# Kernel optimization log

Hardware: AMD Instinct MI355X
Metric: run time of the kernel (lower is better)

The kernel has to match this reference:

```python
import jax, jax.numpy as jnp
import numpy as np

N, E, F_IN = 50000, 1_600_000, 256
HID, HEADS, NCLS = 8, 8, 16  # conv1: 8 heads x 8 dims (concat=64); conv2: 1 head -> 16 classes


def setup_inputs() -> dict:
    key = jax.random.key(0)
    ks = jax.random.split(key, 11)
    x = jax.random.normal(ks[0], (N, F_IN), dtype=jnp.float32)
    edge_index = jax.random.randint(ks[1], (2, E), 0, N, dtype=jnp.int32)
    s1 = 1.0 / np.sqrt(F_IN)
    W1 = jax.random.normal(ks[2], (F_IN, HEADS * HID), jnp.float32) * s1
    a_src1 = jax.random.normal(ks[3], (HEADS, HID), jnp.float32) * 0.1
    a_dst1 = jax.random.normal(ks[4], (HEADS, HID), jnp.float32) * 0.1
    b1 = jnp.zeros((HEADS * HID,), jnp.float32)
    s2 = 1.0 / np.sqrt(HEADS * HID)
    W2 = jax.random.normal(ks[5], (HEADS * HID, NCLS), jnp.float32) * s2
    a_src2 = jax.random.normal(ks[6], (1, NCLS), jnp.float32) * 0.1
    a_dst2 = jax.random.normal(ks[7], (1, NCLS), jnp.float32) * 0.1
    b2 = jnp.zeros((NCLS,), jnp.float32)
    return {"x": x, "edge_index": edge_index, "W1": W1, "a_src1": a_src1,
            "a_dst1": a_dst1, "b1": b1, "W2": W2, "a_src2": a_src2,
            "a_dst2": a_dst2, "b2": b2}


def _gat_conv(x, W, a_src, a_dst, bias, src, dst, n, heads, ch, concat):
    # per-head linear transform: [n, heads, ch]
    h = (x @ W).reshape(n, heads, ch)
    # additive attention logits per node, per head
    al_s = jnp.einsum('nhc,hc->nh', h, a_src)
    al_d = jnp.einsum('nhc,hc->nh', h, a_dst)
    e = jax.nn.leaky_relu(al_s[src] + al_d[dst], 0.2)  # [E_tot, heads]
    # segment softmax grouped by destination node (self-loops guarantee non-empty segments)
    m = jax.ops.segment_max(e, dst, num_segments=n)
    ex = jnp.exp(e - m[dst])
    den = jax.ops.segment_sum(ex, dst, num_segments=n)
    alpha = ex / den[dst]  # [E_tot, heads]
    # scatter-aggregate weighted neighbor features
    out = jax.ops.segment_sum(h[src] * alpha[:, :, None], dst, num_segments=n)
    out = out.reshape(n, heads * ch) if concat else out.mean(axis=1)
    return out + bias


def reference(x, edge_index, W1, a_src1, a_dst1, b1, W2, a_src2, a_dst2, b2):
    # add self-loops (PyG GATConv default)
    loops = jnp.arange(N, dtype=edge_index.dtype)
    src = jnp.concatenate([edge_index[0], loops])
    dst = jnp.concatenate([edge_index[1], loops])
    h = _gat_conv(x, W1, a_src1, a_dst1, b1, src, dst, N, HEADS, HID, True)
    h = jax.nn.elu(h)
    out = _gat_conv(h, W2, a_src2, a_dst2, b2, src, dst, N, 1, NCLS, False)
    return jax.nn.log_softmax(out, axis=1)
```

## Files before the change

### kernel.cpp

```cpp
#include <hip/hip_runtime.h>
#include <hip/hip_fp16.h>

#define NN   50000
#define FIN  256
#define C1   64
#define NH   8
#define NC   16
#define NE   1600000
#define NTOT (NE + NN)

#define CH   256
#define EPC  ((NTOT + CH - 1) / CH)
#define NCB  196
#define GB1  ((NN + 63) / 64)

typedef _Float16 half8 __attribute__((ext_vector_type(8)));
typedef _Float16 half4 __attribute__((ext_vector_type(4)));
typedef float f32x4 __attribute__((ext_vector_type(4)));

#define OFF_H1H   0
#define OFF_H2H   1600000
#define OFF_ALS2  2000000
#define OFF_ALD2  2050000
#define OFF_STAGE 3200000
#define OFF_ALS1  6400000
#define OFF_ALD1  6800000
#define OFF_HM    7200000
#define OFF_BASEK 7251000
#define OFF_BBASE 7302000
#define OFF_OFFS  7302400
#define OFF_SRC   7352500

__global__ __launch_bounds__(256) void k_g1rh(const float* __restrict__ x,
                                              const float* __restrict__ W1,
                                              const float* __restrict__ as1,
                                              const float* __restrict__ ad1,
                                              __half* __restrict__ h1h,
                                              float* __restrict__ als,
                                              float* __restrict__ ald,
                                              const int* __restrict__ ei,
                                              int* __restrict__ H) {
    __shared__ _Float16 wsT[64][264];
    __shared__ _Float16 xs[64][40];
    __shared__ int lh[NCB];
    const int tid = threadIdx.x;

    if (blockIdx.x >= GB1) {
        int k = blockIdx.x - GB1;
        for (int i = tid; i < NCB; i += 256) lh[i] = 0;
        __syncthreads();
        int e0 = k * EPC, e1 = min(e0 + EPC, NTOT);
        for (int e = e0 + tid; e < e1; e += 256) {
            int d = (e < NE) ? ei[NE + e] : (e - NE);
            atomicAdd(&lh[d >> 8], 1);
        }
        __syncthreads();
        for (int i = tid; i < NCB; i += 256) H[k * NCB + i] = lh[i];
        return;
    }

    const int r0 = blockIdx.x * 64;
    {
        int c = tid & 63, kb = tid >> 6;
        #pragma unroll
        for (int j = 0; j < 8; ++j) {
            int k8 = kb + 4 * j;
            half8 hv;
            #pragma unroll
            for (int u = 0; u < 8; ++u)
                hv[u] = (_Float16)W1[(size_t)(k8 * 8 + u) * C1 + c];
            *(half8*)(&wsT[c][k8 * 8]) = hv;
        }
    }

    const int lane = tid & 63;
    const int wv   = tid >> 6;
    const int colb = lane & 15;
    const int rgrp = lane >> 4;
    f32x4 acc[4] = {};
    const int srow = tid >> 2;
    const int sq   = tid & 3;
    for (int k0 = 0; k0 < FIN; k0 += 32) {
        __syncthreads();
        {
            int grow = r0 + srow;
            float4 v0 = make_float4(0.f,0.f,0.f,0.f), v1 = v0;
            if (grow < NN) {
                const float4* xp = (const float4*)(&x[(size_t)grow * FIN + k0 + sq * 8]);
                v0 = xp[0]; v1 = xp[1];
            }
            half8 hv;
            hv[0]=(_Float16)v0.x; hv[1]=(_Float16)v0.y; hv[2]=(_Float16)v0.z; hv[3]=(_Float16)v0.w;
            hv[4]=(_Float16)v1.x; hv[5]=(_Float16)v1.y; hv[6]=(_Float16)v1.z; hv[7]=(_Float16)v1.w;
            *(half8*)(&xs[srow][sq * 8]) = hv;
        }
        __syncthreads();
        half8 a = *(half8*)(&xs[wv * 16 + colb][rgrp * 8]);
        #pragma unroll
        for (int ct = 0; ct < 4; ++ct) {
            half8 b = *(half8*)(&wsT[ct * 16 + colb][k0 + rgrp * 8]);
            acc[ct] = __builtin_amdgcn_mfma_f32_16x16x32_f16(a, b, acc[ct], 0, 0, 0);
        }
    }

    float a_s[4], a_d[4];
    #pragma unroll
    for (int ct = 0; ct < 4; ++ct) { a_s[ct] = as1[ct * 16 + colb]; a_d[ct] = ad1[ct * 16 + colb]; }
    #pragma unroll
    for (int j = 0; j < 4; ++j) {
        int row = r0 + wv * 16 + rgrp * 4 + j;
        bool rv = row < NN;
        #pragma unroll
        for (int ct = 0; ct < 4; ++ct) {
            if (rv) h1h[(size_t)row * C1 + ct * 16 + colb] = __float2half(acc[ct][j]);
            float p = acc[ct][j] * a_s[ct];
            p += __shfl_xor(p, 1); p += __shfl_xor(p, 2); p += __shfl_xor(p, 4);
            float q = acc[ct][j] * a_d[ct];
            q += __shfl_xor(q, 1); q += __shfl_xor(q, 2); q += __shfl_xor(q, 4);
            if (rv && (lane & 7) == 0) {
                int head = ct * 2 + (colb >> 3);
                als[row * NH + head] = p;
                ald[row * NH + head] = q;
            }
        }
    }
}

__global__ __launch_bounds__(256) void k_rsA(const int* __restrict__ H,
                                             int* __restrict__ basek,
                                             int* __restrict__ btot) {
    __shared__ int sc[CH];
    int b = blockIdx.x, t = threadIdx.x;
    int v = H[t * NCB + b];
    sc[t] = v;
    __syncthreads();
    for (int s = 1; s < CH; s <<= 1) {
        int u = (t >= s) ? sc[t - s] : 0;
        __syncthreads();
        sc[t] += u;
        __syncthreads();
    }
    basek[b * CH + t] = sc[t] - v;
    if (t == CH - 1) btot[b] = sc[t];
}

__global__ __launch_bounds__(64) void k_rsB(int* __restrict__ btot,
                                            int* __restrict__ bbase,
                                            int* __restrict__ offs) {
    if (threadIdx.x == 0) {
        int run = 0;
        for (int b = 0; b < NCB; ++b) {
            bbase[b] = run;
            run += btot[b];
        }
        bbase[NCB] = run;
        offs[NN] = NTOT;
    }
}

__global__ __launch_bounds__(256) void k_rscatter(const int* __restrict__ ei,
                                                  const int* __restrict__ basek,
                                                  const int* __restrict__ bbase,
                                                  int* __restrict__ stage) {
    __shared__ int lcur[NCB];
    int k = blockIdx.x;
    for (int i = threadIdx.x; i < NCB; i += 256)
        lcur[i] = bbase[i] + basek[i * CH + k];
    __syncthreads();
    int e0 = k * EPC, e1 = min(e0 + EPC, NTOT);
    for (int e = e0 + threadIdx.x; e < e1; e += 256) {
        int s, d;
        if (e < NE) { s = ei[e]; d = ei[NE + e]; }
        else        { s = e - NE; d = s; }
        int pos = atomicAdd(&lcur[d >> 8], 1);
        stage[pos] = (s << 8) | (d & 255);
    }
}

__global__ __launch_bounds__(256) void k_fsort(const int* __restrict__ stage,
                                               const int* __restrict__ bbase,
                                               int* __restrict__ offs,
                                               int* __restrict__ ssrc) {
    __shared__ int lc[256];
    __shared__ int ls[256];
    __shared__ int lcur[256];
    int b = blockIdx.x, t = threadIdx.x;
    int base = bbase[b];
    int n = bbase[b + 1] - base;
    lc[t] = 0;
    __syncthreads();
    const int* sp = &stage[base];
    for (int i = t; i < n; i += 256) atomicAdd(&lc[sp[i] & 255], 1);
    __syncthreads();
    int v = lc[t];
    ls[t] = v;
    __syncthreads();
    for (int s = 1; s < 256; s <<= 1) {
        int u = (t >= s) ? ls[t - s] : 0;
        __syncthreads();
        ls[t] += u;
        __syncthreads();
    }
    int excl = ls[t] - v;
    int d = b * 256 + t;
    if (d < NN) offs[d] = base + excl;
    lcur[t] = base + excl;
    __syncthreads();
    for (int i = t; i < n; i += 256) {
        int u = sp[i];
        int pos = atomicAdd(&lcur[u & 255], 1);
        ssrc[pos] = u >> 8;
    }
}

__global__ __launch_bounds__(256) void k_agg1(const int* __restrict__ offs,
                                              const int* __restrict__ src,
                                              const __half* __restrict__ h1h,
                                              const float* __restrict__ als,
                                              const float* __restrict__ ald,
                                              const float* __restrict__ b1,
                                              const float* __restrict__ W2,
                                              const float* __restrict__ as2,
                                              const float* __restrict__ ad2,
                                              __half* __restrict__ h2h,
                                              float* __restrict__ als2,
                                              float* __restrict__ ald2) {
    __shared__ float lds_w2[C1][17];
    __shared__ float lds_g[4][C1];
    int tid = threadIdx.x;
    #pragma unroll
    for (int i = tid; i < C1 * NC; i += 256) lds_w2[i >> 4][i & 15] = W2[i];
    __syncthreads();

    int wv = tid >> 6;
    int d = blockIdx.x * 4 + wv;
    if (d >= NN) return;
    const int l  = tid & 63;
    const int q  = l >> 4, lc = l & 15;
    const int hg = lc >> 1;
    const int sub = l >> 3, hw = l & 7;
    const int lane_a = (q << 3) | hg;
    const int lane_b = lane_a + 32;
    int beg = offs[d], end = offs[d + 1];
    float aldv = ald[d * NH + hw];
    f32x4 acc = {0.f, 0.f, 0.f, 0.f};
    float den = 0.f;

    for (int r = beg; r < end; r += 16) {
        int e0 = r + sub, e1 = e0 + 8;
        bool v0 = e0 < end, v1 = e1 < end;
        int s0 = src[v0 ? e0 : end - 1];
        int s1 = src[v1 ? e1 : end - 1];
        float lg0 = als[s0 * NH + hw] + aldv;
        float lg1 = als[s1 * NH + hw] + aldv;
        lg0 = lg0 > 0.f ? lg0 : 0.2f * lg0;
        lg1 = lg1 > 0.f ? lg1 : 0.2f * lg1;
        float w0 = v0 ? __expf(lg0) : 0.f;
        float w1 = v1 ? __expf(lg1) : 0.f;
        #pragma unroll
        for (int i = 0; i < 4; ++i) {
            int srcl = (i & 1) ? lane_b : lane_a;
            int sv   = __shfl((i < 2) ? s0 : s1, srcl);
            float wvv= __shfl((i < 2) ? w0 : w1, srcl);
            half4 hv = *(const half4*)(&h1h[(size_t)sv * C1 + 4 * lc]);
            acc[0] += wvv * (float)hv[0];
            acc[1] += wvv * (float)hv[1];
            acc[2] += wvv * (float)hv[2];
            acc[3] += wvv * (float)hv[3];
            den += wvv;
        }
    }
    #pragma unroll
    for (int k = 0; k < 4; ++k) {
        acc[k] += __shfl_xor(acc[k], 16);
        acc[k] += __shfl_xor(acc[k], 32);
    }
    den += __shfl_xor(den, 16);
    den += __shfl_xor(den, 32);

    float g[4];
    #pragma unroll
    for (int k = 0; k < 4; ++k) {
        float o = acc[k] / den + b1[4 * lc + k];
        g[k] = o > 0.f ? o : (__expf(o) - 1.f);
    }
    if (q == 0) *(float4*)(&lds_g[wv][4 * lc]) = make_float4(g[0], g[1], g[2], g[3]);
    float h2p = 0.f;
    #pragma unroll
    for (int m = 0; m < 16; ++m)
        h2p += lds_g[wv][q * 16 + m] * lds_w2[q * 16 + m][lc];
    h2p += __shfl_xor(h2p, 16);
    h2p += __shfl_xor(h2p, 32);
    if (l < 16) h2h[(size_t)d * NC + lc] = __float2half(h2p);
    float ps = h2p * as2[lc], pd = h2p * ad2[lc];
    ps += __shfl_xor(ps, 1); ps += __shfl_xor(ps, 2);
    ps += __shfl_xor(ps, 4); ps += __shfl_xor(ps, 8);
    pd += __shfl_xor(pd, 1); pd += __shfl_xor(pd, 2);
    pd += __shfl_xor(pd, 4); pd += __shfl_xor(pd, 8);
    if (l == 0) { als2[d] = ps; ald2[d] = pd; }
}

__global__ __launch_bounds__(256) void k_agg2(const int* __restrict__ offs,
                                              const int* __restrict__ src,
                                              const __half* __restrict__ h2h,
                                              const float* __restrict__ als2,
                                              const float* __restrict__ ald2,
                                              const float* __restrict__ b2,
                                              float* __restrict__ out) {
    int d = blockIdx.x * 16 + (threadIdx.x >> 4);
    if (d >= NN) return;
    int c = threadIdx.x & 15;
    int beg = offs[d], end = offs[d + 1];
    float aldv = ald2[d];
    float acc = 0.f, den = 0.f;
    for (int r = beg; r < end; r += 4) {
        int e1 = r + 1, e2 = r + 2, e3 = r + 3;
        bool v1 = e1 < end, v2 = e2 < end, v3 = e3 < end;
        int s0 = src[r];
        int s1 = src[v1 ? e1 : end - 1];
        int s2 = src[v2 ? e2 : end - 1];
        int s3 = src[v3 ? e3 : end - 1];
        float l0 = als2[s0] + aldv;
        float l1 = als2[s1] + aldv;
        float l2 = als2[s2] + aldv;
        float l3 = als2[s3] + aldv;
        l0 = l0 > 0.f ? l0 : 0.2f * l0;
        l1 = l1 > 0.f ? l1 : 0.2f * l1;
        l2 = l2 > 0.f ? l2 : 0.2f * l2;
        l3 = l3 > 0.f ? l3 : 0.2f * l3;
        float w0 = __expf(l0);
        float w1 = v1 ? __expf(l1) : 0.f;
        float w2 = v2 ? __expf(l2) : 0.f;
        float w3 = v3 ? __expf(l3) : 0.f;
        float f0 = __half2float(h2h[(size_t)s0 * NC + c]);
        float f1 = __half2float(h2h[(size_t)s1 * NC + c]);
        float f2 = __half2float(h2h[(size_t)s2 * NC + c]);
        float f3 = __half2float(h2h[(size_t)s3 * NC + c]);
        acc += w0 * f0 + w1 * f1 + w2 * f2 + w3 * f3;
        den += w0 + w1 + w2 + w3;
    }
    float o = acc / den + b2[c];
    float m = o;
    #pragma unroll
    for (int w = 1; w < 16; w <<= 1) m = fmaxf(m, __shfl_xor(m, w));
    float ex = __expf(o - m);
    float sm = ex;
    #pragma unroll
    for (int w = 1; w < 16; w <<= 1) sm += __shfl_xor(sm, w);
    out[(size_t)d * NC + c] = o - m - __logf(sm);
}

extern "C" void kernel_launch(void* const* d_in, const int* in_sizes, int n_in,
                              void* d_out, int out_size, void* d_ws, size_t ws_size,
                              hipStream_t stream) {
    const float* x   = (const float*)d_in[0];
    const int*   ei  = (const int*)  d_in[1];
    const float* W1  = (const float*)d_in[2];
    const float* as1 = (const float*)d_in[3];
    const float* ad1 = (const float*)d_in[4];
    const float* b1  = (const float*)d_in[5];
    const float* W2  = (const float*)d_in[6];
    const float* as2 = (const float*)d_in[7];
    const float* ad2 = (const float*)d_in[8];
    const float* b2  = (const float*)d_in[9];
    float* ws  = (float*)d_ws;
    float* out = (float*)d_out;

    __half* h1h = (__half*)(ws + OFF_H1H);
    __half* h2h = (__half*)(ws + OFF_H2H);
    float* als1 = ws + OFF_ALS1;
    float* ald1 = ws + OFF_ALD1;
    float* als2 = ws + OFF_ALS2;
    float* ald2 = ws + OFF_ALD2;
    int* H      = (int*)(ws + OFF_HM);
    int* basek  = (int*)(ws + OFF_BASEK);
    int* bbase  = (int*)(ws + OFF_BBASE);
    int* offs   = (int*)(ws + OFF_OFFS);
    int* ssrc   = (int*)(ws + OFF_SRC);
    int* stage  = (int*)(ws + OFF_STAGE);

    k_g1rh    <<<GB1 + CH,       256, 0, stream>>>(x, W1, as1, ad1, h1h, als1, ald1, ei, H);
    k_rsA     <<<NCB,            256, 0, stream>>>(H, basek, bbase + NCB + 2 );
    k_rsB     <<<1,               64, 0, stream>>>(bbase + NCB + 2, bbase, offs);
    k_rscatter<<<CH,             256, 0, stream>>>(ei, basek, bbase, stage);
    k_fsort   <<<NCB,            256, 0, stream>>>(stage, bbase, offs, ssrc);
    k_agg1    <<<(NN + 3) / 4,   256, 0, stream>>>(offs, ssrc, h1h, als1, ald1, b1,
                                                   W2, as2, ad2, h2h, als2, ald2);
    k_agg2    <<<(NN + 15) / 16, 256, 0, stream>>>(offs, ssrc, h2h, als2, ald2, b2, out);
}
```

Measured before the change: 142.7 us.

## Split layer-2 GEMM out of agg1 and stage full x tile in LDS

The layer-1 aggregation kernel no longer computes the layer-2 projection. It writes ELU activations in fp16 to a new buffer, and a separate k_gemm2 kernel computes h2 and the layer-2 attention logits. The first GEMM kernel now loads the whole 64x256 x tile into LDS up front instead of looping over k-chunks with two barriers each. This trims LDS use and barriers in agg1 and removes per-iteration syncs in the GEMM, but adds an extra launch plus an activation round trip through memory. It also raises LDS per block in k_g1rh, which can lower occupancy.

```diff
diff --git a/kernel.cpp b/kernel.cpp
--- a/kernel.cpp
+++ b/kernel.cpp
@@ -19,10 +19,11 @@
 typedef float f32x4 __attribute__((ext_vector_type(4)));
 
 #define OFF_H1H   0
-#define OFF_H2H   1600000
-#define OFF_ALS2  2000000
-#define OFF_ALD2  2050000
+#define OFF_G1H   1600000
 #define OFF_STAGE 3200000
+#define OFF_H2H   3200000
+#define OFF_ALS2  3600000
+#define OFF_ALD2  3650000
 #define OFF_ALS1  6400000
 #define OFF_ALD1  6800000
 #define OFF_HM    7200000
@@ -41,11 +42,11 @@
                                               const int* __restrict__ ei,
                                               int* __restrict__ H) {
     __shared__ _Float16 wsT[64][264];
-    __shared__ _Float16 xs[64][40];
-    __shared__ int lh[NCB];
+    __shared__ _Float16 xs[64][264];
     const int tid = threadIdx.x;
 
     if (blockIdx.x >= GB1) {
+        __shared__ int lh[NCB];
         int k = blockIdx.x - GB1;
         for (int i = tid; i < NCB; i += 256) lh[i] = 0;
         __syncthreads();
@@ -72,33 +73,35 @@
             *(half8*)(&wsT[c][k8 * 8]) = hv;
         }
     }
+    {
+        int row = tid >> 2, cb = (tid & 3) * 64;
+        int grow = r0 + row;
+        #pragma unroll
+        for (int j = 0; j < 8; ++j) {
+            float4 v0 = make_float4(0.f,0.f,0.f,0.f), v1 = v0;
+            if (grow < NN) {
+                const float4* xp = (const float4*)(&x[(size_t)grow * FIN + cb + j * 8]);
+                v0 = xp[0]; v1 = xp[1];
+            }
+            half8 hv;
+            hv[0]=(_Float16)v0.x; hv[1]=(_Float16)v0.y; hv[2]=(_Float16)v0.z; hv[3]=(_Float16)v0.w;
+            hv[4]=(_Float16)v1.x; hv[5]=(_Float16)v1.y; hv[6]=(_Float16)v1.z; hv[7]=(_Float16)v1.w;
+            *(half8*)(&xs[row][cb + j * 8]) = hv;
+        }
+    }
+    __syncthreads();
 
     const int lane = tid & 63;
     const int wv   = tid >> 6;
     const int colb = lane & 15;
     const int rgrp = lane >> 4;
     f32x4 acc[4] = {};
-    const int srow = tid >> 2;
-    const int sq   = tid & 3;
-    for (int k0 = 0; k0 < FIN; k0 += 32) {
-        __syncthreads();
-        {
-            int grow = r0 + srow;
-            float4 v0 = make_float4(0.f,0.f,0.f,0.f), v1 = v0;
-            if (grow < NN) {
-                const float4* xp = (const float4*)(&x[(size_t)grow * FIN + k0 + sq * 8]);
-                v0 = xp[0]; v1 = xp[1];
-            }
-            half8 hv;
-            hv[0]=(_Float16)v0.x; hv[1]=(_Float16)v0.y; hv[2]=(_Float16)v0.z; hv[3]=(_Float16)v0.w;
-            hv[4]=(_Float16)v1.x; hv[5]=(_Float16)v1.y; hv[6]=(_Float16)v1.z; hv[7]=(_Float16)v1.w;
-            *(half8*)(&xs[srow][sq * 8]) = hv;
-        }
-        __syncthreads();
-        half8 a = *(half8*)(&xs[wv * 16 + colb][rgrp * 8]);
+    #pragma unroll
+    for (int s = 0; s < 8; ++s) {
+        half8 a = *(half8*)(&xs[wv * 16 + colb][s * 32 + rgrp * 8]);
         #pragma unroll
         for (int ct = 0; ct < 4; ++ct) {
-            half8 b = *(half8*)(&wsT[ct * 16 + colb][k0 + rgrp * 8]);
+            half8 b = *(half8*)(&wsT[ct * 16 + colb][s * 32 + rgrp * 8]);
             acc[ct] = __builtin_amdgcn_mfma_f32_16x16x32_f16(a, b, acc[ct], 0, 0, 0);
         }
     }
@@ -219,23 +222,10 @@
                                               const float* __restrict__ als,
                                               const float* __restrict__ ald,
                                               const float* __restrict__ b1,
-                                              const float* __restrict__ W2,
-                                              const float* __restrict__ as2,
-                                              const float* __restrict__ ad2,
-                                              __half* __restrict__ h2h,
-                                              float* __restrict__ als2,
-                                              float* __restrict__ ald2) {
-    __shared__ float lds_w2[C1][17];
-    __shared__ float lds_g[4][C1];
-    int tid = threadIdx.x;
-    #pragma unroll
-    for (int i = tid; i < C1 * NC; i += 256) lds_w2[i >> 4][i & 15] = W2[i];
-    __syncthreads();
-
-    int wv = tid >> 6;
-    int d = blockIdx.x * 4 + wv;
+                                              _Float16* __restrict__ g1h) {
+    int d = blockIdx.x * 4 + (threadIdx.x >> 6);
     if (d >= NN) return;
-    const int l  = tid & 63;
+    const int l  = threadIdx.x & 63;
     const int q  = l >> 4, lc = l & 15;
     const int hg = lc >> 1;
     const int sub = l >> 3, hw = l & 7;
@@ -277,32 +267,51 @@
     }
     den += __shfl_xor(den, 16);
     den += __shfl_xor(den, 32);
-
-    float g[4];
-    #pragma unroll
-    for (int k = 0; k < 4; ++k) {
-        float o = acc[k] / den + b1[4 * lc + k];
-        g[k] = o > 0.f ? o : (__expf(o) - 1.f);
-    }
-    if (q == 0) *(float4*)(&lds_g[wv][4 * lc]) = make_float4(g[0], g[1], g[2], g[3]);
-    float h2p = 0.f;
-    #pragma unroll
-    for (int m = 0; m < 16; ++m)
-        h2p += lds_g[wv][q * 16 + m] * lds_w2[q * 16 + m][lc];
-    h2p += __shfl_xor(h2p, 16);
-    h2p += __shfl_xor(h2p, 32);
-    if (l < 16) h2h[(size_t)d * NC + lc] = __float2half(h2p);
-    float ps = h2p * as2[lc], pd = h2p * ad2[lc];
-    ps += __shfl_xor(ps, 1); ps += __shfl_xor(ps, 2);
-    ps += __shfl_xor(ps, 4); ps += __shfl_xor(ps, 8);
-    pd += __shfl_xor(pd, 1); pd += __shfl_xor(pd, 2);
-    pd += __shfl_xor(pd, 4); pd += __shfl_xor(pd, 8);
-    if (l == 0) { als2[d] = ps; ald2[d] = pd; }
+    if (q == 0) {
+        half4 gv;
+        #pragma unroll
+        for (int k = 0; k < 4; ++k) {
+            float o = acc[k] / den + b1[4 * lc + k];
+            o = o > 0.f ? o : (__expf(o) - 1.f);
+            gv[k] = (_Float16)o;
+        }
+        *(half4*)(&g1h[(size_t)d * C1 + 4 * lc]) = gv;
+    }
+}
+
+__global__ __launch_bounds__(256) void k_gemm2(const _Float16* __restrict__ g1h,
+                                               const float* __restrict__ W2,
+                                               const float* __restrict__ as2,
+                                               const float* __restrict__ ad2,
+                                               _Float16* __restrict__ h2h,
+                                               float* __restrict__ als2,
+                                               float* __restrict__ ald2) {
+    __shared__ float w2s[C1][17];
+    __shared__ _Float16 hact[16][C1 + 8];
+    int tid = threadIdx.x;
+    for (int i = tid; i < C1 * NC; i += 256) w2s[i >> 4][i & 15] = W2[i];
+    int ln = tid >> 4, j = tid & 15;
+    int n = blockIdx.x * 16 + ln;
+    if (n < NN)
+        *(half4*)(&hact[ln][j * 4]) = *(const half4*)(&g1h[(size_t)n * C1 + j * 4]);
+    __syncthreads();
+    if (n >= NN) return;
+    float sum = 0.f;
+    #pragma unroll
+    for (int c = 0; c < C1; ++c) sum += (float)hact[ln][c] * w2s[c][j];
+    h2h[(size_t)n * NC + j] = (_Float16)sum;
+    float ps = sum * as2[j], pd = sum * ad2[j];
+    #pragma unroll
+    for (int w = 1; w < 16; w <<= 1) {
+        ps += __shfl_xor(ps, w);
+        pd += __shfl_xor(pd, w);
+    }
+    if (j == 0) { als2[n] = ps; ald2[n] = pd; }
 }
 
 __global__ __launch_bounds__(256) void k_agg2(const int* __restrict__ offs,
                                               const int* __restrict__ src,
-                                              const __half* __restrict__ h2h,
+                                              const _Float16* __restrict__ h2h,
                                               const float* __restrict__ als2,
                                               const float* __restrict__ ald2,
                                               const float* __restrict__ b2,
@@ -332,10 +341,10 @@
         float w1 = v1 ? __expf(l1) : 0.f;
         float w2 = v2 ? __expf(l2) : 0.f;
         float w3 = v3 ? __expf(l3) : 0.f;
-        float f0 = __half2float(h2h[(size_t)s0 * NC + c]);
-        float f1 = __half2float(h2h[(size_t)s1 * NC + c]);
-        float f2 = __half2float(h2h[(size_t)s2 * NC + c]);
-        float f3 = __half2float(h2h[(size_t)s3 * NC + c]);
+        float f0 = (float)h2h[(size_t)s0 * NC + c];
+        float f1 = (float)h2h[(size_t)s1 * NC + c];
+        float f2 = (float)h2h[(size_t)s2 * NC + c];
+        float f3 = (float)h2h[(size_t)s3 * NC + c];
         acc += w0 * f0 + w1 * f1 + w2 * f2 + w3 * f3;
         den += w0 + w1 + w2 + w3;
     }
@@ -366,8 +375,9 @@
     float* ws  = (float*)d_ws;
     float* out = (float*)d_out;
 
-    __half* h1h = (__half*)(ws + OFF_H1H);
-    __half* h2h = (__half*)(ws + OFF_H2H);
+    __half*    h1h  = (__half*)(ws + OFF_H1H);
+    _Float16*  g1h  = (_Float16*)(ws + OFF_G1H);
+    _Float16*  h2h  = (_Float16*)(ws + OFF_H2H);
     float* als1 = ws + OFF_ALS1;
     float* ald1 = ws + OFF_ALD1;
     float* als2 = ws + OFF_ALS2;
@@ -384,7 +394,7 @@
     k_rsB     <<<1,               64, 0, stream>>>(bbase + NCB + 2, bbase, offs);
     k_rscatter<<<CH,             256, 0, stream>>>(ei, basek, bbase, stage);
     k_fsort   <<<NCB,            256, 0, stream>>>(stage, bbase, offs, ssrc);
-    k_agg1    <<<(NN + 3) / 4,   256, 0, stream>>>(offs, ssrc, h1h, als1, ald1, b1,
-                                                   W2, as2, ad2, h2h, als2, ald2);
+    k_agg1    <<<(NN + 3) / 4,   256, 0, stream>>>(offs, ssrc, h1h, als1, ald1, b1, g1h);
+    k_gemm2   <<<(NN + 15) / 16, 256, 0, stream>>>(g1h, W2, as2, ad2, h2h, als2, ald2);
     k_agg2    <<<(NN + 15) / 16, 256, 0, stream>>>(offs, ssrc, h2h, als2, ald2, b2, out);
 }
```

New measurement: 146.3 us. +2.6%, slower.
